# Kernel optimization log

Measured on AMD Instinct MI355X. Metric: run time of the kernel, lower is better.

## Reference

```python
import jax, jax.numpy as jnp
import numpy as np
from jax import lax

B, S = 32, 256
V, D = 32000, 300   # pretrained word embeddings
P, PD = 35, 32      # pos vocab / pos embed dim (from source)
M = 66              # morph feature dim
H = 6               # LSTM units per direction -> bilstm_output_size = 12
A = 12


def _lstm(x, Wx, Wh, b, reverse=False):
    # x: [B,S,F] -> h: [B,S,H]; keras gate order i,f,c,o
    xg = x @ Wx + b  # precompute input projection once: [B,S,4H]
    def step(carry, xt):
        h, c = carry
        g = xt + h @ Wh
        i, f, cand, o = jnp.split(g, 4, axis=-1)
        c = jax.nn.sigmoid(f) * c + jax.nn.sigmoid(i) * jnp.tanh(cand)
        h = jax.nn.sigmoid(o) * jnp.tanh(c)
        return (h, c), h
    h0 = jnp.zeros((x.shape[0], Wh.shape[0]), x.dtype)
    _, hs = lax.scan(step, (h0, h0), jnp.swapaxes(xg, 0, 1), reverse=reverse)
    return jnp.swapaxes(hs, 0, 1)


def setup_inputs() -> dict:
    key = jax.random.key(0)
    ks = jax.random.split(key, 16)
    F = D + PD + M
    n = lambda k, shp, s=0.1: jax.random.normal(k, shp, dtype=jnp.float32) * s
    return {
        'words': jax.random.randint(ks[0], (B, S), 0, V),
        'pos': jax.random.randint(ks[1], (B, S), 0, P),
        'morph': jax.random.uniform(ks[2], (B, S, M), dtype=jnp.float32),
        'heads': jax.random.randint(ks[3], (B, S), 0, S),
        'word_table': n(ks[4], (V, D)),
        'pos_table': n(ks[5], (P, PD)),
        'Wx_f': n(ks[6], (F, 4 * H)), 'Wh_f': n(ks[7], (H, 4 * H)), 'b_f': jnp.zeros((4 * H,), jnp.float32),
        'Wx_b': n(ks[8], (F, 4 * H)), 'Wh_b': n(ks[9], (H, 4 * H)), 'b_b': jnp.zeros((4 * H,), jnp.float32),
        'Wu': n(ks[10], (A, A)), 'bu': jnp.zeros((A,), jnp.float32),
        'Ww': n(ks[11], (A, A)), 'bw': jnp.zeros((A,), jnp.float32),
        'v': n(ks[12], (A,)),
    }


def reference(words, pos, morph, heads, word_table, pos_table,
              Wx_f, Wh_f, b_f, Wx_b, Wh_b, b_b, Wu, bu, Ww, bw, v):
    # embed + concat -> [B,S,F]
    feats = jnp.concatenate([word_table[words], pos_table[pos], morph], axis=-1)
    # BiLSTM encoder -> [B,S,12] (dropout disabled / eval)
    hf = _lstm(feats, Wx_f, Wh_f, b_f)
    hb = _lstm(feats, Wx_b, Wh_b, b_b, reverse=True)
    repr_ = jnp.concatenate([hf, hb], axis=-1)
    # Bahdanau arc scoring, vectorized over dependant i (the tf loop):
    # scores[b,i,j] = v . tanh(u_a(repr)[b,j] + w_a(repr)[b,i])
    ua = repr_ @ Wu + bu  # head-position term (j)
    wa = repr_ @ Ww + bw  # dependant term (i)
    scores = jnp.einsum('bijd,d->bij', jnp.tanh(ua[:, None, :, :] + wa[:, :, None, :]), v)
    # the equality-based mask in tf picks out j == i (self cannot be head)
    eye = jnp.eye(S, dtype=bool)
    scores = jnp.where(eye[None], -10000.0, scores)
    # per-step sparse CE (from_logits, mean over batch), summed over i=1..S-1
    logp = jax.nn.log_softmax(scores, axis=-1)
    ce = -jnp.take_along_axis(logp, heads[:, :, None], axis=2)[..., 0]  # [B,S]
    loss = jnp.sum(jnp.mean(ce[:, 1:], axis=0))
    # parent_prob_table: exp(scores) concatenated along axis 0, i-major as in tf loop
    table = jnp.swapaxes(jnp.exp(scores[:, 1:, :]), 0, 1).reshape((S - 1) * B, S)
    return loss, table
```

## Files before the change

### kernel.cpp

```cpp
#include <hip/hip_runtime.h>
#include <hip/hip_bf16.h>

#define BB 32
#define SS 256
#define DD 300
#define PDD 32
#define MM 66
#define FF 398
#define HH 6
#define G4 24
#define AA 12
#define L2E 1.4426950408889634f

__device__ __forceinline__ float fast_rcp(float x) { return __builtin_amdgcn_rcpf(x); }
__device__ __forceinline__ float fast_tanh(float x) {
    return 1.f - 2.f * fast_rcp(__expf(2.f * x) + 1.f);
}
__device__ __forceinline__ float bcast_lane(float x, int l) {
    return __int_as_float(__builtin_amdgcn_readlane(__float_as_int(x), l));
}
template<int CTRL>
__device__ __forceinline__ float quad_bcast(float v) {
    return __int_as_float(__builtin_amdgcn_mov_dpp(__float_as_int(v), CTRL, 0xf, 0xf, true));
}

#define EPB 32
__global__ __launch_bounds__(256) void k_embed_proj(
    const int* __restrict__ words, const int* __restrict__ pos,
    const float* __restrict__ morph, const float* __restrict__ wtab,
    const float* __restrict__ ptab,
    const float* __restrict__ Wxf, const float* __restrict__ bfv,
    const float* __restrict__ Wxb, const float* __restrict__ bbv,
    float* __restrict__ xgf, float* __restrict__ xgb)
{
    __shared__ float4 sF[100][33];
    __shared__ float4 sW[48 * 100];
    int t  = threadIdx.x;
    int p0 = blockIdx.x * EPB;

    for (int idx = t; idx < EPB * 75; idx += 256) {
        int p = idx / 75, q = idx % 75;
        sF[q][p] = *(const float4*)(wtab + (size_t)words[p0 + p] * DD + 4 * q);
    }
    {
        int idx = t;
        int p = idx / 8, q = idx % 8;
        sF[75 + q][p] = *(const float4*)(ptab + pos[p0 + p] * PDD + 4 * q);
    }
    for (int idx = t; idx < EPB * 17; idx += 256) {
        int p = idx / 17, mq = idx % 17;
        const float2* ms = (const float2*)(morph + (size_t)(p0 + p) * MM);
        float2 lo = ms[2 * mq];
        float2 hi = (mq < 16) ? ms[2 * mq + 1] : make_float2(0.f, 0.f);
        sF[83 + mq][p] = make_float4(lo.x, lo.y, hi.x, hi.y);
    }
    {
        float* sWf = (float*)sW;
        for (int idx = t; idx < FF * G4; idx += 256) {
            int k = idx / G4, j = idx % G4;
            sWf[j * 400 + k]        = Wxf[idx];
            sWf[(24 + j) * 400 + k] = Wxb[idx];
        }
        if (t < 2 * G4) {
            int j = t >> 1, k = 398 + (t & 1);
            sWf[j * 400 + k] = 0.f; sWf[(24 + j) * 400 + k] = 0.f;
        }
    }
    __syncthreads();

    int lane = t & 63, w = t >> 6;
    int p    = lane & 31;
    int cg   = w * 2 + (lane >> 5);
    int dir  = cg >> 2;
    int tg   = cg & 3;
    int j0   = tg * 6;
    const float4* wc = sW + (dir * 24 + j0) * 100;

    float a0 = 0.f, a1 = 0.f, a2 = 0.f, a3 = 0.f, a4 = 0.f, a5 = 0.f;
    #pragma unroll 4
    for (int q = 0; q < 100; ++q) {
        float4 f = sF[q][p];
        float4 w0 = wc[0 * 100 + q], w1 = wc[1 * 100 + q], w2 = wc[2 * 100 + q];
        float4 w3 = wc[3 * 100 + q], w4 = wc[4 * 100 + q], w5 = wc[5 * 100 + q];
        a0 = fmaf(f.x, w0.x, a0); a0 = fmaf(f.y, w0.y, a0);
        a0 = fmaf(f.z, w0.z, a0); a0 = fmaf(f.w, w0.w, a0);
        a1 = fmaf(f.x, w1.x, a1); a1 = fmaf(f.y, w1.y, a1);
        a1 = fmaf(f.z, w1.z, a1); a1 = fmaf(f.w, w1.w, a1);
        a2 = fmaf(f.x, w2.x, a2); a2 = fmaf(f.y, w2.y, a2);
        a2 = fmaf(f.z, w2.z, a2); a2 = fmaf(f.w, w2.w, a2);
        a3 = fmaf(f.x, w3.x, a3); a3 = fmaf(f.y, w3.y, a3);
        a3 = fmaf(f.z, w3.z, a3); a3 = fmaf(f.w, w3.w, a3);
        a4 = fmaf(f.x, w4.x, a4); a4 = fmaf(f.y, w4.y, a4);
        a4 = fmaf(f.z, w4.z, a4); a4 = fmaf(f.w, w4.w, a4);
        a5 = fmaf(f.x, w5.x, a5); a5 = fmaf(f.y, w5.y, a5);
        a5 = fmaf(f.z, w5.z, a5); a5 = fmaf(f.w, w5.w, a5);
    }

    float kk = (tg == 2) ? 2.f * L2E : -L2E;
    const float* bias = dir ? bbv : bfv;
    float* o = (dir ? xgb : xgf) + (size_t)(p0 + p) * G4 + j0;
    o[0] = (a0 + bias[j0 + 0]) * kk; o[1] = (a1 + bias[j0 + 1]) * kk;
    o[2] = (a2 + bias[j0 + 2]) * kk; o[3] = (a3 + bias[j0 + 3]) * kk;
    o[4] = (a4 + bias[j0 + 4]) * kk; o[5] = (a5 + bias[j0 + 5]) * kk;
}

__global__ __launch_bounds__(64) void k_lstm(
    const float* __restrict__ xgf, const float* __restrict__ xgb,
    const float* __restrict__ Whf, const float* __restrict__ Whb,
    float* __restrict__ repr)
{
    __shared__ float sxg[(SS + 8) * G4];
    __shared__ float hbuf[SS * HH];
    int blk = blockIdx.x;
    int dir = blk >> 5;
    int b   = blk & 31;
    int lane = threadIdx.x;

    const float* xg = (dir ? xgb : xgf) + (size_t)b * SS * G4;
    const float* Wh = dir ? Whb : Whf;

    {
        const float4* src = (const float4*)xg;
        float4* dst = (float4*)sxg;
        #pragma unroll
        for (int u = 0; u < 24; ++u) {
            int d = lane + u * 64;
            int row = d / 6, c4 = d - row * 6;
            int drow = dir ? (SS - 1 - row) : row;
            dst[drow * 6 + c4] = src[d];
        }
        for (int g2 = lane; g2 < 8 * G4; g2 += 64) sxg[SS * G4 + g2] = 0.f;
    }

    int g    = lane % G4;
    int cell = g >> 2;
    int type = g & 3;
    int j    = type * HH + cell;

    float kk = (type == 2) ? 2.f * L2E : -L2E;
    float wh[HH];
    #pragma unroll
    for (int m = 0; m < HH; ++m) wh[m] = Wh[m * G4 + j] * kk;
    float Bc = (type == 2) ? 1.f : 0.f;
    float Ac = (type == 2) ? -1.f : 1.f;

    float sh[HH];
    #pragma unroll
    for (int m = 0; m < HH; ++m) sh[m] = 0.f;
    float c = 0.f;
    bool wr = (lane < G4) && ((lane & 3) == 0);
    __syncthreads();

    const float* xb = sxg + j;

    float pg[4];
    #pragma unroll
    for (int sl = 0; sl < 4; ++sl) pg[sl] = xb[sl * G4];

    #pragma unroll 1
    for (int t = 0; t < SS; t += 4) {
        #pragma unroll
        for (int sl = 0; sl < 4; ++sl) {
            float x = pg[sl];
            pg[sl] = xb[(t + 4 + sl) * G4];

            float aa  = fmaf(sh[1], wh[1], fmaf(sh[0], wh[0], x));
            float bb2 = fmaf(sh[3], wh[3], sh[2] * wh[2]);
            float cc2 = fmaf(sh[5], wh[5], sh[4] * wh[4]);
            x = (aa + bb2) + cc2;

            float e   = __builtin_amdgcn_exp2f(x);
            float val = fmaf(Bc, e, Ac) * fast_rcp(1.f + e);

            float vi = quad_bcast<0>(val);
            float vf = quad_bcast<85>(val);
            float vc = quad_bcast<170>(val);
            float vo = quad_bcast<255>(val);

            c = fmaf(vf, c, vi * vc);
            float ec = __builtin_amdgcn_exp2f(c * (2.f * L2E));
            float h  = (ec - 1.f) * fast_rcp(ec + 1.f) * vo;

            if (wr) hbuf[(t + sl) * HH + cell] = h;
            #pragma unroll
            for (int m = 0; m < HH; ++m) sh[m] = bcast_lane(h, 4 * m);
        }
    }
    __syncthreads();

    #pragma unroll
    for (int u = 0; u < (SS * HH) / 64; ++u) {
        int idx = lane + u * 64;
        int tt = idx / 6, cc = idx - tt * 6;
        int s = dir ? (SS - 1 - tt) : tt;
        repr[((size_t)b * SS + s) * (2 * HH) + dir * HH + cc] = hbuf[idx];
    }
}

__global__ __launch_bounds__(256) void k_uawa(
    const float* __restrict__ repr,
    const float* __restrict__ Wu, const float* __restrict__ bu,
    const float* __restrict__ Ww, const float* __restrict__ bw,
    float* __restrict__ ua, float* __restrict__ wa)
{
    int bs = blockIdx.x * blockDim.x + threadIdx.x;
    float r[AA];
    #pragma unroll
    for (int e = 0; e < AA; ++e) r[e] = repr[(size_t)bs * AA + e];
    #pragma unroll
    for (int d = 0; d < AA; ++d) {
        float au = bu[d], aw = bw[d];
        #pragma unroll
        for (int e = 0; e < AA; ++e) {
            au = fmaf(r[e], Wu[e * AA + d], au);
            aw = fmaf(r[e], Ww[e * AA + d], aw);
        }
        ua[(size_t)bs * AA + d] = au;
        wa[(size_t)bs * AA + d] = aw;
    }
}

__global__ __launch_bounds__(256) void k_score(
    const float* __restrict__ ua, const float* __restrict__ wa,
    const float* __restrict__ v, const int* __restrict__ heads,
    float* __restrict__ out, float* __restrict__ ce)
{
    int bi = blockIdx.x;
    int i  = bi & 255;
    int j  = threadIdx.x;

    __shared__ float swa[AA], sv[AA];
    if (j < AA) { swa[j] = wa[(size_t)bi * AA + j]; sv[j] = v[j]; }
    __syncthreads();

    const float* uj = ua + ((size_t)(bi & ~255) + j) * AA;
    float s = 0.f;
    #pragma unroll
    for (int d = 0; d < AA; ++d) s = fmaf(sv[d], fast_tanh(uj[d] + swa[d]), s);
    if (j == i) s = -10000.f;

    float e = __expf(s);
    if (i >= 1)
        out[1 + (((size_t)(i - 1) * BB + (bi >> 8)) * SS + j)] = e;

    float r = e;
    #pragma unroll
    for (int off = 32; off > 0; off >>= 1) r += __shfl_xor(r, off, 64);
    __shared__ float part[4];
    if ((j & 63) == 0) part[j >> 6] = r;
    __syncthreads();
    float tot = part[0] + part[1] + part[2] + part[3];

    if (j == heads[bi])
        ce[bi] = (i >= 1) ? (__logf(tot) - s) : 0.f;
}

__global__ __launch_bounds__(256) void k_loss(const float* __restrict__ ce,
                                              float* __restrict__ out)
{
    __shared__ float red[256];
    int t = threadIdx.x;
    float a = 0.f;
    for (int k = t; k < BB * SS; k += 256) a += ce[k];
    red[t] = a; __syncthreads();
    for (int off = 128; off > 0; off >>= 1) {
        if (t < off) red[t] += red[t + off];
        __syncthreads();
    }
    if (t == 0) out[0] = red[0] * (1.f / BB);
}

extern "C" void kernel_launch(void* const* d_in, const int* in_sizes, int n_in,
                              void* d_out, int out_size, void* d_ws, size_t ws_size,
                              hipStream_t stream)
{
    const int*   words = (const int*)  d_in[0];
    const int*   pos   = (const int*)  d_in[1];
    const float* morph = (const float*)d_in[2];
    const int*   heads = (const int*)  d_in[3];
    const float* wtab  = (const float*)d_in[4];
    const float* ptab  = (const float*)d_in[5];
    const float* Wxf   = (const float*)d_in[6];
    const float* Whf   = (const float*)d_in[7];
    const float* bf    = (const float*)d_in[8];
    const float* Wxb   = (const float*)d_in[9];
    const float* Whb   = (const float*)d_in[10];
    const float* bb    = (const float*)d_in[11];
    const float* Wu    = (const float*)d_in[12];
    const float* bu    = (const float*)d_in[13];
    const float* Ww    = (const float*)d_in[14];
    const float* bw    = (const float*)d_in[15];
    const float* v     = (const float*)d_in[16];
    float* out = (float*)d_out;

    float* xgf   = (float*)d_ws;
    float* xgb   = xgf   + (size_t)BB*SS*G4;
    float* repr  = xgb   + (size_t)BB*SS*G4;
    float* ua    = repr  + (size_t)BB*SS*2*HH;
    float* wa    = ua    + (size_t)BB*SS*AA;
    float* ce    = wa    + (size_t)BB*SS*AA;

    k_embed_proj<<<(BB * SS) / EPB, 256, 0, stream>>>(words, pos, morph, wtab, ptab,
                                                      Wxf, bf, Wxb, bb, xgf, xgb);
    k_lstm<<<BB * 2, 64, 0, stream>>>(xgf, xgb, Whf, Whb, repr);
    k_uawa<<<(BB * SS) / 256, 256, 0, stream>>>(repr, Wu, bu, Ww, bw, ua, wa);
    k_score<<<BB * SS, 256, 0, stream>>>(ua, wa, v, heads, out, ce);
    k_loss<<<1, 256, 0, stream>>>(ce, out);
}
```

Baseline: 73.80 us.

## Split input projection over K halves, pretranspose weights, fold bias into LSTM load

Adds a small kernel that transposes the input weights once into global memory, so each projection block no longer restages the full weight matrix into shared memory. The projection kernel now splits the feature dimension into two halves across blocks, writes two partial sums, and uses 64 positions per 512-thread block. The LSTM kernel sums the partials, adds the bias and applies the gate scaling while loading into shared memory, and writes h straight to repr instead of going through a shared buffer. This trades one extra launch and extra workspace traffic for less redundant weight staging and more parallelism in the projection.

After: 83.83 us. +13.6%, slower.

```diff
diff --git a/kernel.cpp b/kernel.cpp
--- a/kernel.cpp
+++ b/kernel.cpp
@@ -24,64 +24,68 @@
     return __int_as_float(__builtin_amdgcn_mov_dpp(__float_as_int(v), CTRL, 0xf, 0xf, true));
 }
 
-#define EPB 32
-__global__ __launch_bounds__(256) void k_embed_proj(
+__global__ __launch_bounds__(256) void k_wtprep(
+    const float* __restrict__ Wxf, const float* __restrict__ Wxb,
+    float* __restrict__ WT)
+{
+    const float* Wx = blockIdx.x ? Wxb : Wxf;
+    float* wt = WT + blockIdx.x * (G4 * 400);
+    for (int idx = threadIdx.x; idx < G4 * 400; idx += 256) {
+        int j = idx / 400, k = idx % 400;
+        wt[idx] = (k < FF) ? Wx[k * G4 + j] : 0.f;
+    }
+}
+
+__global__ __launch_bounds__(512) void k_xg(
     const int* __restrict__ words, const int* __restrict__ pos,
     const float* __restrict__ morph, const float* __restrict__ wtab,
-    const float* __restrict__ ptab,
-    const float* __restrict__ Wxf, const float* __restrict__ bfv,
-    const float* __restrict__ Wxb, const float* __restrict__ bbv,
-    float* __restrict__ xgf, float* __restrict__ xgb)
-{
-    __shared__ float4 sF[100][33];
-    __shared__ float4 sW[48 * 100];
+    const float* __restrict__ ptab, const float* __restrict__ WT,
+    float* __restrict__ xgp0, float* __restrict__ xgp1)
+{
+    __shared__ float4 sF[50][66];
     int t  = threadIdx.x;
-    int p0 = blockIdx.x * EPB;
-
-    for (int idx = t; idx < EPB * 75; idx += 256) {
-        int p = idx / 75, q = idx % 75;
-        sF[q][p] = *(const float4*)(wtab + (size_t)words[p0 + p] * DD + 4 * q);
-    }
-    {
-        int idx = t;
-        int p = idx / 8, q = idx % 8;
-        sF[75 + q][p] = *(const float4*)(ptab + pos[p0 + p] * PDD + 4 * q);
-    }
-    for (int idx = t; idx < EPB * 17; idx += 256) {
-        int p = idx / 17, mq = idx % 17;
-        const float2* ms = (const float2*)(morph + (size_t)(p0 + p) * MM);
-        float2 lo = ms[2 * mq];
-        float2 hi = (mq < 16) ? ms[2 * mq + 1] : make_float2(0.f, 0.f);
-        sF[83 + mq][p] = make_float4(lo.x, lo.y, hi.x, hi.y);
-    }
-    {
-        float* sWf = (float*)sW;
-        for (int idx = t; idx < FF * G4; idx += 256) {
-            int k = idx / G4, j = idx % G4;
-            sWf[j * 400 + k]        = Wxf[idx];
-            sWf[(24 + j) * 400 + k] = Wxb[idx];
-        }
-        if (t < 2 * G4) {
-            int j = t >> 1, k = 398 + (t & 1);
-            sWf[j * 400 + k] = 0.f; sWf[(24 + j) * 400 + k] = 0.f;
+    int kh = blockIdx.x & 1;
+    int p0 = (blockIdx.x >> 1) * 64;
+
+    if (kh == 0) {
+        for (int idx = t; idx < 64 * 50; idx += 512) {
+            int p = idx / 50, q = idx % 50;
+            sF[q][p] = *(const float4*)(wtab + (size_t)words[p0 + p] * DD + 4 * q);
+        }
+    } else {
+        for (int idx = t; idx < 64 * 25; idx += 512) {
+            int p = idx / 25, q = idx % 25;
+            sF[q][p] = *(const float4*)(wtab + (size_t)words[p0 + p] * DD + 200 + 4 * q);
+        }
+        for (int idx = t; idx < 64 * 8; idx += 512) {
+            int p = idx / 8, q = idx % 8;
+            sF[25 + q][p] = *(const float4*)(ptab + pos[p0 + p] * PDD + 4 * q);
+        }
+        for (int idx = t; idx < 64 * 34; idx += 512) {
+            int p = idx / 34, m = idx % 34;
+            const float2* ms = (const float2*)(morph + (size_t)(p0 + p) * MM);
+            float2 v = (m < 33) ? ms[m] : make_float2(0.f, 0.f);
+            *(float2*)((float*)&sF[33 + (m >> 1)][p] + 2 * (m & 1)) = v;
         }
     }
     __syncthreads();
 
-    int lane = t & 63, w = t >> 6;
-    int p    = lane & 31;
-    int cg   = w * 2 + (lane >> 5);
+    int lane = t & 63;
+    int cg   = __builtin_amdgcn_readfirstlane(t >> 6);
     int dir  = cg >> 2;
-    int tg   = cg & 3;
-    int j0   = tg * 6;
-    const float4* wc = sW + (dir * 24 + j0) * 100;
+    int j0   = (cg & 3) * 6;
+    const float* wb = WT + (dir * G4 + j0) * 400 + kh * 200;
 
     float a0 = 0.f, a1 = 0.f, a2 = 0.f, a3 = 0.f, a4 = 0.f, a5 = 0.f;
-    #pragma unroll 4
-    for (int q = 0; q < 100; ++q) {
-        float4 f = sF[q][p];
-        float4 w0 = wc[0 * 100 + q], w1 = wc[1 * 100 + q], w2 = wc[2 * 100 + q];
-        float4 w3 = wc[3 * 100 + q], w4 = wc[4 * 100 + q], w5 = wc[5 * 100 + q];
+    #pragma unroll 2
+    for (int q = 0; q < 50; ++q) {
+        float4 f  = sF[q][lane];
+        float4 w0 = *(const float4*)(wb + 0 * 400 + 4 * q);
+        float4 w1 = *(const float4*)(wb + 1 * 400 + 4 * q);
+        float4 w2 = *(const float4*)(wb + 2 * 400 + 4 * q);
+        float4 w3 = *(const float4*)(wb + 3 * 400 + 4 * q);
+        float4 w4 = *(const float4*)(wb + 4 * 400 + 4 * q);
+        float4 w5 = *(const float4*)(wb + 5 * 400 + 4 * q);
         a0 = fmaf(f.x, w0.x, a0); a0 = fmaf(f.y, w0.y, a0);
         a0 = fmaf(f.z, w0.z, a0); a0 = fmaf(f.w, w0.w, a0);
         a1 = fmaf(f.x, w1.x, a1); a1 = fmaf(f.y, w1.y, a1);
@@ -96,38 +100,45 @@
         a5 = fmaf(f.z, w5.z, a5); a5 = fmaf(f.w, w5.w, a5);
     }
 
-    float kk = (tg == 2) ? 2.f * L2E : -L2E;
-    const float* bias = dir ? bbv : bfv;
-    float* o = (dir ? xgb : xgf) + (size_t)(p0 + p) * G4 + j0;
-    o[0] = (a0 + bias[j0 + 0]) * kk; o[1] = (a1 + bias[j0 + 1]) * kk;
-    o[2] = (a2 + bias[j0 + 2]) * kk; o[3] = (a3 + bias[j0 + 3]) * kk;
-    o[4] = (a4 + bias[j0 + 4]) * kk; o[5] = (a5 + bias[j0 + 5]) * kk;
+    float* o = (kh ? xgp1 : xgp0) +
+               ((size_t)dir * BB * SS + p0 + lane) * G4 + j0;
+    ((float2*)o)[0] = make_float2(a0, a1);
+    ((float2*)o)[1] = make_float2(a2, a3);
+    ((float2*)o)[2] = make_float2(a4, a5);
 }
 
 __global__ __launch_bounds__(64) void k_lstm(
-    const float* __restrict__ xgf, const float* __restrict__ xgb,
+    const float* __restrict__ xgp0, const float* __restrict__ xgp1,
+    const float* __restrict__ bfv, const float* __restrict__ bbv,
     const float* __restrict__ Whf, const float* __restrict__ Whb,
     float* __restrict__ repr)
 {
     __shared__ float sxg[(SS + 8) * G4];
-    __shared__ float hbuf[SS * HH];
     int blk = blockIdx.x;
     int dir = blk >> 5;
     int b   = blk & 31;
     int lane = threadIdx.x;
 
-    const float* xg = (dir ? xgb : xgf) + (size_t)b * SS * G4;
+    const float4* s0 = (const float4*)(xgp0 + ((size_t)dir * BB * SS + b * SS) * G4);
+    const float4* s1 = (const float4*)(xgp1 + ((size_t)dir * BB * SS + b * SS) * G4);
+    const float4* bias4 = (const float4*)(dir ? bbv : bfv);
     const float* Wh = dir ? Whb : Whf;
 
     {
-        const float4* src = (const float4*)xg;
         float4* dst = (float4*)sxg;
         #pragma unroll
         for (int u = 0; u < 24; ++u) {
             int d = lane + u * 64;
             int row = d / 6, c4 = d - row * 6;
             int drow = dir ? (SS - 1 - row) : row;
-            dst[drow * 6 + c4] = src[d];
+            float4 v0 = s0[d], v1 = s1[d], bv = bias4[c4];
+            int cb = c4 * 4;
+            float4 v;
+            v.x = (v0.x + v1.x + bv.x) * ((cb + 0 >= 12 && cb + 0 < 18) ? 2.f * L2E : -L2E);
+            v.y = (v0.y + v1.y + bv.y) * ((cb + 1 >= 12 && cb + 1 < 18) ? 2.f * L2E : -L2E);
+            v.z = (v0.z + v1.z + bv.z) * ((cb + 2 >= 12 && cb + 2 < 18) ? 2.f * L2E : -L2E);
+            v.w = (v0.w + v1.w + bv.w) * ((cb + 3 >= 12 && cb + 3 < 18) ? 2.f * L2E : -L2E);
+            dst[drow * 6 + c4] = v;
         }
         for (int g2 = lane; g2 < 8 * G4; g2 += 64) sxg[SS * G4 + g2] = 0.f;
     }
@@ -152,6 +163,7 @@
     __syncthreads();
 
     const float* xb = sxg + j;
+    float* rb = repr + (size_t)b * SS * (2 * HH) + dir * HH + cell;
 
     float pg[4];
     #pragma unroll
@@ -181,19 +193,12 @@
             float ec = __builtin_amdgcn_exp2f(c * (2.f * L2E));
             float h  = (ec - 1.f) * fast_rcp(ec + 1.f) * vo;
 
-            if (wr) hbuf[(t + sl) * HH + cell] = h;
+            int tt = t + sl;
+            int s  = dir ? (SS - 1 - tt) : tt;
+            if (wr) rb[(size_t)s * (2 * HH)] = h;
             #pragma unroll
             for (int m = 0; m < HH; ++m) sh[m] = bcast_lane(h, 4 * m);
         }
-    }
-    __syncthreads();
-
-    #pragma unroll
-    for (int u = 0; u < (SS * HH) / 64; ++u) {
-        int idx = lane + u * 64;
-        int tt = idx / 6, cc = idx - tt * 6;
-        int s = dir ? (SS - 1 - tt) : tt;
-        repr[((size_t)b * SS + s) * (2 * HH) + dir * HH + cc] = hbuf[idx];
     }
 }
 
@@ -293,16 +298,17 @@
     const float* v     = (const float*)d_in[16];
     float* out = (float*)d_out;
 
-    float* xgf   = (float*)d_ws;
-    float* xgb   = xgf   + (size_t)BB*SS*G4;
-    float* repr  = xgb   + (size_t)BB*SS*G4;
-    float* ua    = repr  + (size_t)BB*SS*2*HH;
-    float* wa    = ua    + (size_t)BB*SS*AA;
-    float* ce    = wa    + (size_t)BB*SS*AA;
-
-    k_embed_proj<<<(BB * SS) / EPB, 256, 0, stream>>>(words, pos, morph, wtab, ptab,
-                                                      Wxf, bf, Wxb, bb, xgf, xgb);
-    k_lstm<<<BB * 2, 64, 0, stream>>>(xgf, xgb, Whf, Whb, repr);
+    float* xgp0 = (float*)d_ws;
+    float* xgp1 = xgp0 + (size_t)2*BB*SS*G4;
+    float* WT   = xgp1 + (size_t)2*BB*SS*G4;
+    float* repr = WT   + (size_t)2*G4*400;
+    float* ua   = repr + (size_t)BB*SS*2*HH;
+    float* wa   = ua   + (size_t)BB*SS*AA;
+    float* ce   = wa   + (size_t)BB*SS*AA;
+
+    k_wtprep<<<2, 256, 0, stream>>>(Wxf, Wxb, WT);
+    k_xg<<<256, 512, 0, stream>>>(words, pos, morph, wtab, ptab, WT, xgp0, xgp1);
+    k_lstm<<<BB * 2, 64, 0, stream>>>(xgp0, xgp1, bf, bb, Whf, Whb, repr);
     k_uawa<<<(BB * SS) / 256, 256, 0, stream>>>(repr, Wu, bu, Ww, bw, ua, wa);
     k_score<<<BB * SS, 256, 0, stream>>>(ua, wa, v, heads, out, ce);
     k_loss<<<1, 256, 0, stream>>>(ce, out);
```

## Interleave two independent LSTM sequences per wavefront to hide recurrence latency

Applied to the files above, without the earlier changes.

Each LSTM block now processes two batch elements (b and b+16) in lockstep, interleaving their serial dependency chains so the exp/rcp/DPP/readlane latencies of one sequence overlap with the other. The grid shrinks from 64 to 32 single-wave blocks. LDS use per block doubles and register pressure rises, and only half as many CUs are used, so any gain depends on the recurrence being latency-bound rather than throughput-bound.

New measurement: 90.69 us. 22.9% more time.

```diff
diff --git a/kernel.cpp b/kernel.cpp
--- a/kernel.cpp
+++ b/kernel.cpp
@@ -109,27 +109,36 @@
     const float* __restrict__ Whf, const float* __restrict__ Whb,
     float* __restrict__ repr)
 {
-    __shared__ float sxg[(SS + 8) * G4];
-    __shared__ float hbuf[SS * HH];
-    int blk = blockIdx.x;
-    int dir = blk >> 5;
-    int b   = blk & 31;
+    __shared__ float sxgA[(SS + 8) * G4];
+    __shared__ float sxgB[(SS + 8) * G4];
+    __shared__ float hbufA[SS * HH];
+    __shared__ float hbufB[SS * HH];
+    int q   = blockIdx.x;
+    int dir = q >> 4;
+    int bA  = q & 15;
+    int bB  = bA + 16;
     int lane = threadIdx.x;
 
-    const float* xg = (dir ? xgb : xgf) + (size_t)b * SS * G4;
+    const float* xgbase = dir ? xgb : xgf;
     const float* Wh = dir ? Whb : Whf;
 
     {
-        const float4* src = (const float4*)xg;
-        float4* dst = (float4*)sxg;
+        const float4* srcA = (const float4*)(xgbase + (size_t)bA * SS * G4);
+        const float4* srcB = (const float4*)(xgbase + (size_t)bB * SS * G4);
+        float4* dA = (float4*)sxgA;
+        float4* dB = (float4*)sxgB;
         #pragma unroll
         for (int u = 0; u < 24; ++u) {
             int d = lane + u * 64;
             int row = d / 6, c4 = d - row * 6;
             int drow = dir ? (SS - 1 - row) : row;
-            dst[drow * 6 + c4] = src[d];
-        }
-        for (int g2 = lane; g2 < 8 * G4; g2 += 64) sxg[SS * G4 + g2] = 0.f;
+            dA[drow * 6 + c4] = srcA[d];
+            dB[drow * 6 + c4] = srcB[d];
+        }
+        for (int g2 = lane; g2 < 8 * G4; g2 += 64) {
+            sxgA[SS * G4 + g2] = 0.f;
+            sxgB[SS * G4 + g2] = 0.f;
+        }
     }
 
     int g    = lane % G4;
@@ -144,46 +153,63 @@
     float Bc = (type == 2) ? 1.f : 0.f;
     float Ac = (type == 2) ? -1.f : 1.f;
 
-    float sh[HH];
-    #pragma unroll
-    for (int m = 0; m < HH; ++m) sh[m] = 0.f;
-    float c = 0.f;
+    float shA[HH], shB[HH];
+    #pragma unroll
+    for (int m = 0; m < HH; ++m) { shA[m] = 0.f; shB[m] = 0.f; }
+    float cA = 0.f, cB = 0.f;
     bool wr = (lane < G4) && ((lane & 3) == 0);
     __syncthreads();
 
-    const float* xb = sxg + j;
-
-    float pg[4];
-    #pragma unroll
-    for (int sl = 0; sl < 4; ++sl) pg[sl] = xb[sl * G4];
+    const float* xbA = sxgA + j;
+    const float* xbB = sxgB + j;
+
+    float pgA[4], pgB[4];
+    #pragma unroll
+    for (int sl = 0; sl < 4; ++sl) { pgA[sl] = xbA[sl * G4]; pgB[sl] = xbB[sl * G4]; }
 
     #pragma unroll 1
     for (int t = 0; t < SS; t += 4) {
         #pragma unroll
         for (int sl = 0; sl < 4; ++sl) {
-            float x = pg[sl];
-            pg[sl] = xb[(t + 4 + sl) * G4];
-
-            float aa  = fmaf(sh[1], wh[1], fmaf(sh[0], wh[0], x));
-            float bb2 = fmaf(sh[3], wh[3], sh[2] * wh[2]);
-            float cc2 = fmaf(sh[5], wh[5], sh[4] * wh[4]);
-            x = (aa + bb2) + cc2;
-
-            float e   = __builtin_amdgcn_exp2f(x);
-            float val = fmaf(Bc, e, Ac) * fast_rcp(1.f + e);
-
-            float vi = quad_bcast<0>(val);
-            float vf = quad_bcast<85>(val);
-            float vc = quad_bcast<170>(val);
-            float vo = quad_bcast<255>(val);
-
-            c = fmaf(vf, c, vi * vc);
-            float ec = __builtin_amdgcn_exp2f(c * (2.f * L2E));
-            float h  = (ec - 1.f) * fast_rcp(ec + 1.f) * vo;
-
-            if (wr) hbuf[(t + sl) * HH + cell] = h;
+            float x1 = pgA[sl], x2 = pgB[sl];
+            pgA[sl] = xbA[(t + 4 + sl) * G4];
+            pgB[sl] = xbB[(t + 4 + sl) * G4];
+
+            float a1 = fmaf(shA[1], wh[1], fmaf(shA[0], wh[0], x1));
+            float a2 = fmaf(shB[1], wh[1], fmaf(shB[0], wh[0], x2));
+            float b1 = fmaf(shA[3], wh[3], shA[2] * wh[2]);
+            float b2 = fmaf(shB[3], wh[3], shB[2] * wh[2]);
+            float d1 = fmaf(shA[5], wh[5], shA[4] * wh[4]);
+            float d2 = fmaf(shB[5], wh[5], shB[4] * wh[4]);
+            x1 = (a1 + b1) + d1;
+            x2 = (a2 + b2) + d2;
+
+            float e1 = __builtin_amdgcn_exp2f(x1);
+            float e2 = __builtin_amdgcn_exp2f(x2);
+            float v1 = fmaf(Bc, e1, Ac) * fast_rcp(1.f + e1);
+            float v2 = fmaf(Bc, e2, Ac) * fast_rcp(1.f + e2);
+
+            float vi1 = quad_bcast<0>(v1),   vi2 = quad_bcast<0>(v2);
+            float vf1 = quad_bcast<85>(v1),  vf2 = quad_bcast<85>(v2);
+            float vc1 = quad_bcast<170>(v1), vc2 = quad_bcast<170>(v2);
+            float vo1 = quad_bcast<255>(v1), vo2 = quad_bcast<255>(v2);
+
+            cA = fmaf(vf1, cA, vi1 * vc1);
+            cB = fmaf(vf2, cB, vi2 * vc2);
+            float ec1 = __builtin_amdgcn_exp2f(cA * (2.f * L2E));
+            float ec2 = __builtin_amdgcn_exp2f(cB * (2.f * L2E));
+            float h1 = (ec1 - 1.f) * fast_rcp(ec1 + 1.f) * vo1;
+            float h2 = (ec2 - 1.f) * fast_rcp(ec2 + 1.f) * vo2;
+
+            if (wr) {
+                hbufA[(t + sl) * HH + cell] = h1;
+                hbufB[(t + sl) * HH + cell] = h2;
+            }
             #pragma unroll
-            for (int m = 0; m < HH; ++m) sh[m] = bcast_lane(h, 4 * m);
+            for (int m = 0; m < HH; ++m) {
+                shA[m] = bcast_lane(h1, 4 * m);
+                shB[m] = bcast_lane(h2, 4 * m);
+            }
         }
     }
     __syncthreads();
@@ -193,7 +219,8 @@
         int idx = lane + u * 64;
         int tt = idx / 6, cc = idx - tt * 6;
         int s = dir ? (SS - 1 - tt) : tt;
-        repr[((size_t)b * SS + s) * (2 * HH) + dir * HH + cc] = hbuf[idx];
+        repr[((size_t)bA * SS + s) * (2 * HH) + dir * HH + cc] = hbufA[idx];
+        repr[((size_t)bB * SS + s) * (2 * HH) + dir * HH + cc] = hbufB[idx];
     }
 }
 
@@ -302,7 +329,7 @@
 
     k_embed_proj<<<(BB * SS) / EPB, 256, 0, stream>>>(words, pos, morph, wtab, ptab,
                                                       Wxf, bf, Wxb, bb, xgf, xgb);
-    k_lstm<<<BB * 2, 64, 0, stream>>>(xgf, xgb, Whf, Whb, repr);
+    k_lstm<<<32, 64, 0, stream>>>(xgf, xgb, Whf, Whb, repr);
     k_uawa<<<(BB * SS) / 256, 256, 0, stream>>>(repr, Wu, bu, Ww, bw, ua, wa);
     k_score<<<BB * SS, 256, 0, stream>>>(ua, wa, v, heads, out, ce);
     k_loss<<<1, 256, 0, stream>>>(ce, out);
```

## Pretranspose Wx in a prep kernel, widen projection blocks, simplify score tanh

Applied to the files above, without the earlier changes.

The input-projection weight transpose moves out of each embedding block into a separate two-block prep kernel that writes to workspace. The projection kernel then reads weights with wave-uniform (scalar-friendly) loads and handles 64 positions with 512 threads, so each block no longer refills shared memory with the weights. The score kernel folds the 2*log2e factor into ua/wa and rewrites the sum of v*tanh as sum(v) minus 2*sum(v/(1+exp2)), with float4 loads. The cost is an extra kernel launch and a global round trip for the transposed weights.

New measurement: 83.93 us. 13.7% more time.

```diff
diff --git a/kernel.cpp b/kernel.cpp
--- a/kernel.cpp
+++ b/kernel.cpp
@@ -13,9 +13,6 @@
 #define L2E 1.4426950408889634f
 
 __device__ __forceinline__ float fast_rcp(float x) { return __builtin_amdgcn_rcpf(x); }
-__device__ __forceinline__ float fast_tanh(float x) {
-    return 1.f - 2.f * fast_rcp(__expf(2.f * x) + 1.f);
-}
 __device__ __forceinline__ float bcast_lane(float x, int l) {
     return __int_as_float(__builtin_amdgcn_readlane(__float_as_int(x), l));
 }
@@ -24,64 +21,67 @@
     return __int_as_float(__builtin_amdgcn_mov_dpp(__float_as_int(v), CTRL, 0xf, 0xf, true));
 }
 
-#define EPB 32
-__global__ __launch_bounds__(256) void k_embed_proj(
+__global__ __launch_bounds__(256) void k_wtprep(
+    const float* __restrict__ Wxf, const float* __restrict__ Wxb,
+    float* __restrict__ WT)
+{
+    const float* Wx = blockIdx.x ? Wxb : Wxf;
+    float* wt = WT + blockIdx.x * (G4 * 400);
+    int t = threadIdx.x;
+    for (int idx = t; idx < FF * G4; idx += 256) {
+        int k = idx / G4, j = idx % G4;
+        wt[j * 400 + k] = Wx[idx];
+    }
+    if (t < 2 * G4) {
+        int j = t >> 1, k = 398 + (t & 1);
+        wt[j * 400 + k] = 0.f;
+    }
+}
+
+__global__ __launch_bounds__(512) void k_xg(
     const int* __restrict__ words, const int* __restrict__ pos,
     const float* __restrict__ morph, const float* __restrict__ wtab,
-    const float* __restrict__ ptab,
-    const float* __restrict__ Wxf, const float* __restrict__ bfv,
-    const float* __restrict__ Wxb, const float* __restrict__ bbv,
+    const float* __restrict__ ptab, const float* __restrict__ WT,
+    const float* __restrict__ bfv, const float* __restrict__ bbv,
     float* __restrict__ xgf, float* __restrict__ xgb)
 {
-    __shared__ float4 sF[100][33];
-    __shared__ float4 sW[48 * 100];
+    __shared__ float4 sF[100][64];
     int t  = threadIdx.x;
-    int p0 = blockIdx.x * EPB;
-
-    for (int idx = t; idx < EPB * 75; idx += 256) {
-        int p = idx / 75, q = idx % 75;
+    int p0 = blockIdx.x * 64;
+
+    for (int idx = t; idx < 64 * 75; idx += 512) {
+        int p = idx & 63, q = idx >> 6;
         sF[q][p] = *(const float4*)(wtab + (size_t)words[p0 + p] * DD + 4 * q);
     }
     {
-        int idx = t;
-        int p = idx / 8, q = idx % 8;
+        int p = t & 63, q = t >> 6;
         sF[75 + q][p] = *(const float4*)(ptab + pos[p0 + p] * PDD + 4 * q);
     }
-    for (int idx = t; idx < EPB * 17; idx += 256) {
-        int p = idx / 17, mq = idx % 17;
+    for (int idx = t; idx < 64 * 34; idx += 512) {
+        int p = idx & 63, m = idx >> 6;
         const float2* ms = (const float2*)(morph + (size_t)(p0 + p) * MM);
-        float2 lo = ms[2 * mq];
-        float2 hi = (mq < 16) ? ms[2 * mq + 1] : make_float2(0.f, 0.f);
-        sF[83 + mq][p] = make_float4(lo.x, lo.y, hi.x, hi.y);
-    }
-    {
-        float* sWf = (float*)sW;
-        for (int idx = t; idx < FF * G4; idx += 256) {
-            int k = idx / G4, j = idx % G4;
-            sWf[j * 400 + k]        = Wxf[idx];
-            sWf[(24 + j) * 400 + k] = Wxb[idx];
-        }
-        if (t < 2 * G4) {
-            int j = t >> 1, k = 398 + (t & 1);
-            sWf[j * 400 + k] = 0.f; sWf[(24 + j) * 400 + k] = 0.f;
-        }
-    }
-    __syncthreads();
-
-    int lane = t & 63, w = t >> 6;
-    int p    = lane & 31;
-    int cg   = w * 2 + (lane >> 5);
-    int dir  = cg >> 2;
-    int tg   = cg & 3;
+        float2 v = (m < 33) ? ms[m] : make_float2(0.f, 0.f);
+        ((float2*)&sF[83 + (m >> 1)][p])[m & 1] = v;
+    }
+    __syncthreads();
+
+    int lane = t & 63;
+    int w    = __builtin_amdgcn_readfirstlane(t >> 6);
+    int dir  = w >> 2;
+    int tg   = w & 3;
     int j0   = tg * 6;
-    const float4* wc = sW + (dir * 24 + j0) * 100;
+    const float* wb = WT + (dir * G4 + j0) * 400;
 
     float a0 = 0.f, a1 = 0.f, a2 = 0.f, a3 = 0.f, a4 = 0.f, a5 = 0.f;
-    #pragma unroll 4
+    #pragma unroll 2
     for (int q = 0; q < 100; ++q) {
-        float4 f = sF[q][p];
-        float4 w0 = wc[0 * 100 + q], w1 = wc[1 * 100 + q], w2 = wc[2 * 100 + q];
-        float4 w3 = wc[3 * 100 + q], w4 = wc[4 * 100 + q], w5 = wc[5 * 100 + q];
+        float4 f  = sF[q][lane];
+        const float4 w0 = *(const float4*)(wb + 0 * 400 + 4 * q);
+        const float4 w1 = *(const float4*)(wb + 1 * 400 + 4 * q);
+        const float4 w2 = *(const float4*)(wb + 2 * 400 + 4 * q);
+        const float4 w3 = *(const float4*)(wb + 3 * 400 + 4 * q);
+        const float4 w4 = *(const float4*)(wb + 4 * 400 + 4 * q);
+        const float4 w5 = *(const float4*)(wb + 5 * 400 + 4 * q);
         a0 = fmaf(f.x, w0.x, a0); a0 = fmaf(f.y, w0.y, a0);
         a0 = fmaf(f.z, w0.z, a0); a0 = fmaf(f.w, w0.w, a0);
         a1 = fmaf(f.x, w1.x, a1); a1 = fmaf(f.y, w1.y, a1);
@@ -98,10 +98,10 @@
 
     float kk = (tg == 2) ? 2.f * L2E : -L2E;
     const float* bias = dir ? bbv : bfv;
-    float* o = (dir ? xgb : xgf) + (size_t)(p0 + p) * G4 + j0;
-    o[0] = (a0 + bias[j0 + 0]) * kk; o[1] = (a1 + bias[j0 + 1]) * kk;
-    o[2] = (a2 + bias[j0 + 2]) * kk; o[3] = (a3 + bias[j0 + 3]) * kk;
-    o[4] = (a4 + bias[j0 + 4]) * kk; o[5] = (a5 + bias[j0 + 5]) * kk;
+    float* o = (dir ? xgb : xgf) + (size_t)(p0 + lane) * G4 + j0;
+    ((float2*)o)[0] = make_float2((a0 + bias[j0 + 0]) * kk, (a1 + bias[j0 + 1]) * kk);
+    ((float2*)o)[1] = make_float2((a2 + bias[j0 + 2]) * kk, (a3 + bias[j0 + 3]) * kk);
+    ((float2*)o)[2] = make_float2((a4 + bias[j0 + 4]) * kk, (a5 + bias[j0 + 5]) * kk);
 }
 
 __global__ __launch_bounds__(64) void k_lstm(
@@ -215,8 +215,8 @@
             au = fmaf(r[e], Wu[e * AA + d], au);
             aw = fmaf(r[e], Ww[e * AA + d], aw);
         }
-        ua[(size_t)bs * AA + d] = au;
-        wa[(size_t)bs * AA + d] = aw;
+        ua[(size_t)bs * AA + d] = au * (2.f * L2E);
+        wa[(size_t)bs * AA + d] = aw * (2.f * L2E);
     }
 }
 
@@ -233,13 +233,26 @@
     if (j < AA) { swa[j] = wa[(size_t)bi * AA + j]; sv[j] = v[j]; }
     __syncthreads();
 
+    float sumv = 0.f;
+    #pragma unroll
+    for (int d = 0; d < AA; ++d) sumv += sv[d];
+
     const float* uj = ua + ((size_t)(bi & ~255) + j) * AA;
-    float s = 0.f;
-    #pragma unroll
-    for (int d = 0; d < AA; ++d) s = fmaf(sv[d], fast_tanh(uj[d] + swa[d]), s);
+    float4 u0 = *(const float4*)(uj);
+    float4 u1 = *(const float4*)(uj + 4);
+    float4 u2 = *(const float4*)(uj + 8);
+    float us[AA] = {u0.x, u0.y, u0.z, u0.w, u1.x, u1.y, u1.z, u1.w,
+                    u2.x, u2.y, u2.z, u2.w};
+    float acc = 0.f;
+    #pragma unroll
+    for (int d = 0; d < AA; ++d) {
+        float e_d = __builtin_amdgcn_exp2f(us[d] + swa[d]);
+        acc = fmaf(sv[d], fast_rcp(1.f + e_d), acc);
+    }
+    float s = fmaf(-2.f, acc, sumv);
     if (j == i) s = -10000.f;
 
-    float e = __expf(s);
+    float e = __builtin_amdgcn_exp2f(s * L2E);
     if (i >= 1)
         out[1 + (((size_t)(i - 1) * BB + (bi >> 8)) * SS + j)] = e;
 
@@ -293,15 +306,17 @@
     const float* v     = (const float*)d_in[16];
     float* out = (float*)d_out;
 
-    float* xgf   = (float*)d_ws;
-    float* xgb   = xgf   + (size_t)BB*SS*G4;
-    float* repr  = xgb   + (size_t)BB*SS*G4;
-    float* ua    = repr  + (size_t)BB*SS*2*HH;
-    float* wa    = ua    + (size_t)BB*SS*AA;
-    float* ce    = wa    + (size_t)BB*SS*AA;
-
-    k_embed_proj<<<(BB * SS) / EPB, 256, 0, stream>>>(words, pos, morph, wtab, ptab,
-                                                      Wxf, bf, Wxb, bb, xgf, xgb);
+    float* xgf  = (float*)d_ws;
+    float* xgb  = xgf  + (size_t)BB*SS*G4;
+    float* repr = xgb  + (size_t)BB*SS*G4;
+    float* ua   = repr + (size_t)BB*SS*2*HH;
+    float* wa   = ua   + (size_t)BB*SS*AA;
+    float* ce   = wa   + (size_t)BB*SS*AA;
+    float* WT   = ce   + (size_t)BB*SS;
+
+    k_wtprep<<<2, 256, 0, stream>>>(Wxf, Wxb, WT);
+    k_xg<<<(BB * SS) / 64, 512, 0, stream>>>(words, pos, morph, wtab, ptab, WT,
+                                             bf, bb, xgf, xgb);
     k_lstm<<<BB * 2, 64, 0, stream>>>(xgf, xgb, Whf, Whb, repr);
     k_uawa<<<(BB * SS) / 256, 256, 0, stream>>>(repr, Wu, bu, Ww, bw, ua, wa);
     k_score<<<BB * SS, 256, 0, stream>>>(ua, wa, v, heads, out, ce);
```
